# Optimization experiments

Hardware: AMD Instinct MI355X
Metric: run time of the kernel (lower is better)

The kernel has to match this reference:

```python
import jax, jax.numpy as jnp
import numpy as np

N = 50000      # nodes
E = 600000     # edges
DIN = 128      # dim_in
DOUT = 128     # dim_out (mulhead=1)
DG = 64        # dim_gate


def setup_inputs() -> dict:
    key = jax.random.key(0)
    ks = jax.random.split(key, 10)
    rows = jax.random.randint(ks[0], (E,), 0, N, dtype=jnp.int32)   # dest nodes
    cols = jax.random.randint(ks[1], (E,), 0, N, dtype=jnp.int32)   # src nodes
    vals = jax.random.uniform(ks[2], (E,), dtype=jnp.float32)       # adj_norm values
    feat = jax.random.normal(ks[3], (N, DIN), dtype=jnp.float32)
    s = 1.0 / np.sqrt(DIN)
    W0 = jax.random.normal(ks[4], (DIN, DOUT), dtype=jnp.float32) * s
    b0 = jnp.zeros((DOUT,), dtype=jnp.float32)
    W1 = jax.random.normal(ks[5], (DIN, DOUT), dtype=jnp.float32) * s
    b1 = jnp.zeros((DOUT,), dtype=jnp.float32)
    att = jax.random.normal(ks[6], (2 * DOUT,), dtype=jnp.float32) * 0.1  # attention param [1, 2*DOUT] flattened
    W_pool = jax.random.normal(ks[7], (DIN, DG), dtype=jnp.float32) * s    # weight_pool_gate
    W_gate = jax.random.normal(ks[8], (2 * DIN + DG, 1), dtype=jnp.float32) * 0.05  # weight_gate, mulhead=1
    offset0 = jnp.zeros((DOUT,), dtype=jnp.float32)
    scale0 = jnp.ones((DOUT,), dtype=jnp.float32)
    offset1 = jnp.zeros((DOUT,), dtype=jnp.float32)
    scale1 = jnp.ones((DOUT,), dtype=jnp.float32)
    return dict(rows=rows, cols=cols, vals=vals, feat=feat, W0=W0, b0=b0,
                W1=W1, b1=b1, att=att, W_pool=W_pool, W_gate=W_gate,
                offset0=offset0, scale0=scale0, offset1=offset1, scale1=scale1)


def _batch_norm(x, scale, offset):
    # per-node norm over the feature dim (unbiased=False), matching _batch_norm
    m = x.mean(axis=1, keepdims=True)
    v = x.var(axis=1, keepdims=True) + 1e-9
    return (x - m) * scale * jax.lax.rsqrt(v) + offset


def reference(rows, cols, vals, feat, W0, b0, W1, b1, att, W_pool, W_gate,
              offset0, scale0, offset1, scale1):
    n = feat.shape[0]
    d = W0.shape[1]
    # --- gate value (GaAN eq. 3) ---
    zj = feat @ W_pool                                   # [N, DG]
    neigh_zj = jax.ops.segment_max(zj[cols], rows, num_segments=n)  # per-row max over neighbors
    neigh_zj = jnp.where(jnp.isfinite(neigh_zj), neigh_zj, 0.0)     # empty rows -> zeros
    neigh_mean = jax.ops.segment_sum(vals[:, None] * feat[cols], rows, num_segments=n)  # spmm(adj, feat)
    gate = jnp.concatenate([feat, neigh_zj, neigh_mean], axis=1) @ W_gate  # [N, 1]
    # --- per-order feature transforms (order=1, mulhead=1) ---
    h0 = jax.nn.relu(feat @ W0 + b0)                     # order 0 (self)
    h1 = jax.nn.relu(feat @ W1 + b1)                     # order 1 (neighbor)
    # --- sparse attention aggregation ---
    a_self = jax.nn.leaky_relu(h0 @ att[:d], 0.2)        # [N]
    a_neigh = jax.nn.leaky_relu(h1 @ att[d:], 0.2)       # [N]
    e = a_self[rows] + a_neigh[cols]                     # per-edge score (replaces adj values)
    agg = jax.ops.segment_sum(e[:, None] * h1[cols], rows, num_segments=n)  # spmm(att_adj, h1)
    agg = agg * gate[:, :1]                              # gated
    # --- per-node batch norm, then 'mean' aggregation (sum of orders) ---
    return _batch_norm(h0, scale0, offset0) + _batch_norm(agg, scale1, offset1)
```

## Files before the change

kernel.cpp:

```cpp
#include <hip/hip_runtime.h>

#define DIN 128
#define DG 64

typedef __attribute__((ext_vector_type(8))) short short8;
typedef __attribute__((ext_vector_type(4))) float f32x4;

static __device__ __forceinline__ unsigned short f2bf(float x) {
    unsigned u = __builtin_bit_cast(unsigned, x);
    u = (u + 0x7FFF + ((u >> 16) & 1)) >> 16;
    return (unsigned short)u;
}
static __device__ __forceinline__ float bf2f(unsigned short s) {
    return __builtin_bit_cast(float, (unsigned)s << 16);
}
static __device__ __forceinline__ float bflo(unsigned u) {
    return __builtin_bit_cast(float, u << 16);
}
static __device__ __forceinline__ float bfhi(unsigned u) {
    return __builtin_bit_cast(float, u & 0xFFFF0000u);
}


#define AS_LD 132
#define ZJ_SMEM 25088

static __device__ __forceinline__ void zj_body(
    const float* __restrict__ feat, const float* __restrict__ Wp,
    const float* __restrict__ Wg,
    float* __restrict__ zjc, float* __restrict__ gpart, float* __restrict__ anf,
    int zb, int N, char* smem) {
    float* As = (float*)smem;
    float* Bs = (float*)(smem + 32 * AS_LD * 4);
    int tid = threadIdx.x;
    int tx = tid & 15, ty = tid >> 4;
    int m0 = zb * 128;
    if (m0 >= N) return;
    float acc[8][4];
    #pragma unroll
    for (int r = 0; r < 8; ++r)
        #pragma unroll
        for (int c = 0; c < 4; ++c) acc[r][c] = 0.f;
    float gdot[8], fdot[8];
    #pragma unroll
    for (int r = 0; r < 8; ++r) { gdot[r] = 0.f; fdot[r] = 0.f; }
    for (int kc = 0; kc < 128; kc += 32) {
        for (int i = tid; i < 1024; i += 256) {
            int m = i >> 3, kq = (i & 7) << 2;
            int node = m0 + m;
            float4 f;
            if (node < N) f = *(const float4*)&feat[(size_t)node * 128 + kc + kq];
            else          f = make_float4(0.f, 0.f, 0.f, 0.f);
            As[(kq + 0) * AS_LD + m] = f.x;
            As[(kq + 1) * AS_LD + m] = f.y;
            As[(kq + 2) * AS_LD + m] = f.z;
            As[(kq + 3) * AS_LD + m] = f.w;
        }
        for (int i = tid; i < 512; i += 256) {
            int k = i >> 4, cq = (i & 15) << 2;
            *(float4*)&Bs[k * 64 + cq] = *(const float4*)&Wp[(size_t)(kc + k) * 64 + cq];
        }
        __syncthreads();
        #pragma unroll 8
        for (int kk = 0; kk < 32; ++kk) {
            const float* ar = &As[kk * AS_LD];
            float4 a0 = *(const float4*)(ar + 4 * tx);
            float4 a1 = *(const float4*)(ar + 64 + 4 * tx);
            float4 b0v = *(const float4*)&Bs[kk * 64 + 4 * ty];
            float a[8] = {a0.x, a0.y, a0.z, a0.w, a1.x, a1.y, a1.z, a1.w};
            #pragma unroll
            for (int r = 0; r < 8; ++r) {
                acc[r][0] += a[r] * b0v.x; acc[r][1] += a[r] * b0v.y;
                acc[r][2] += a[r] * b0v.z; acc[r][3] += a[r] * b0v.w;
            }
            float g1 = Wg[kc + kk];
            float g2 = Wg[192 + kc + kk];
            #pragma unroll
            for (int r = 0; r < 8; ++r) { gdot[r] += a[r] * g1; fdot[r] += a[r] * g2; }
        }
        __syncthreads();
    }
    #pragma unroll
    for (int r = 0; r < 8; ++r) {
        int node = m0 + ((r < 4) ? (4 * tx + r) : (64 + 4 * tx + (r - 4)));
        if (node >= N) continue;
        *(float4*)&zjc[(size_t)node * 64 + 4 * ty] =
            make_float4(acc[r][0], acc[r][1], acc[r][2], acc[r][3]);
        if (ty == 0) { gpart[node] = gdot[r]; anf[2 * (size_t)node + 1] = fdot[r]; }
    }
}

__global__ void k_pre(const int* __restrict__ rows, int* __restrict__ deg,
                      int* __restrict__ slot, int E, int nDeg,
                      const float* __restrict__ W0, const float* __restrict__ W1,
                      unsigned short* __restrict__ Bt,
                      const float* __restrict__ feat, const float* __restrict__ Wp,
                      const float* __restrict__ Wg,
                      float* __restrict__ zjc, float* __restrict__ gpart,
                      float* __restrict__ anf, int N) {
    __shared__ __align__(16) char smem[ZJ_SMEM];
    int b = blockIdx.x;
    if (b < nDeg) {
        int e = b * 256 + threadIdx.x;
        if (e < E) slot[e] = atomicAdd(&deg[rows[e]], 1);
        return;
    }
    if (b < nDeg + 128) {
        int k = b - nDeg;
        int c = threadIdx.x;
        const float* W = (c < 128) ? W0 : W1;
        Bt[c * 128 + k] = f2bf(W[k * 128 + (c & 127)]);
        return;
    }
    zj_body(feat, Wp, Wg, zjc, gpart, anf, b - nDeg - 128, N, smem);
}

#define ALD 136
#define RED_OFF 32768
#define SMEM_BYTES 33792

static __device__ __forceinline__ void mfma_body(
    const float* __restrict__ feat, const unsigned short* __restrict__ Bt,
    const float* __restrict__ b0, const float* __restrict__ b1,
    const float* __restrict__ att, const float* __restrict__ zjc,
    float* __restrict__ h0, char* __restrict__ pack,
    float* __restrict__ anf, float* __restrict__ a_self, int N, char* smem) {
    unsigned short* Ah = (unsigned short*)smem;
    float* sredA = (float*)(smem + RED_OFF);
    float* nredA = sredA + 128;
    char* pb = smem;
    int tid = threadIdx.x;
    int m0 = blockIdx.x * 64;
    for (int i = tid; i < 2048; i += 256) {
        int row = i >> 5, ch = i & 31;
        int node = m0 + row;
        float4 f;
        if (node < N) f = *(const float4*)&feat[(size_t)node * 128 + ch * 4];
        else          f = make_float4(0.f, 0.f, 0.f, 0.f);
        unsigned p0 = (unsigned)f2bf(f.x) | ((unsigned)f2bf(f.y) << 16);
        unsigned p1 = (unsigned)f2bf(f.z) | ((unsigned)f2bf(f.w) << 16);
        *(uint2*)&Ah[row * ALD + ch * 4] = make_uint2(p0, p1);
    }
    __syncthreads();
    int w = tid >> 6, lane = tid & 63;
    int lm = lane & 15, q = lane >> 4;
    f32x4 acc[4][4];
    #pragma unroll
    for (int rt = 0; rt < 4; ++rt)
        #pragma unroll
        for (int ct = 0; ct < 4; ++ct)
            #pragma unroll
            for (int r = 0; r < 4; ++r) acc[rt][ct][r] = 0.f;
    #pragma unroll
    for (int ks = 0; ks < 4; ++ks) {
        short8 a[4], b[4];
        #pragma unroll
        for (int rt = 0; rt < 4; ++rt)
            a[rt] = *(const short8*)&Ah[(rt * 16 + lm) * ALD + ks * 32 + q * 8];
        #pragma unroll
        for (int ct = 0; ct < 4; ++ct)
            b[ct] = *(const short8*)&Bt[(size_t)(w * 64 + ct * 16 + lm) * 128 + ks * 32 + q * 8];
        #pragma unroll
        for (int rt = 0; rt < 4; ++rt)
            #pragma unroll
            for (int ct = 0; ct < 4; ++ct)
                acc[rt][ct] = __builtin_amdgcn_mfma_f32_16x16x32_bf16(a[rt], b[ct], acc[rt][ct], 0, 0, 0);
    }
    __syncthreads();

    float sacc[4][4];
    #pragma unroll
    for (int rt = 0; rt < 4; ++rt)
        #pragma unroll
        for (int r = 0; r < 4; ++r) sacc[rt][r] = 0.f;
    #pragma unroll
    for (int ct = 0; ct < 4; ++ct) {
        int col = w * 64 + ct * 16 + lm;
        float attc = att[col];
        float bias = (w < 2) ? b0[col] : b1[col - 128];
        int cp = col - 128;
        int pofs = (cp >> 2) * 16 + (cp & 3) * 2;
        #pragma unroll
        for (int rt = 0; rt < 4; ++rt) {
            #pragma unroll
            for (int r = 0; r < 4; ++r) {
                float v = acc[rt][ct][r] + bias;
                v = fmaxf(v, 0.f);
                sacc[rt][r] += v * attc;
                int row = rt * 16 + q * 4 + r;
                if (w < 2) {
                    int node = m0 + row;
                    if (node < N) h0[(size_t)node * 128 + col] = v;
                } else {
                    *(unsigned short*)(pb + row * 512 + pofs) = f2bf(v);
                }
            }
        }
    }
    for (int i = tid; i < 1024; i += 256) {
        int row = i >> 4, cq = i & 15;
        int node = m0 + row;
        float4 z;
        if (node < N) z = *(const float4*)&zjc[(size_t)node * 64 + cq * 4];
        else          z = make_float4(0.f, 0.f, 0.f, 0.f);
        char* prow = pb + row * 512 + cq * 32 + 8;
        *(float2*)(prow)      = make_float2(z.x, z.y);
        *(float2*)(prow + 16) = make_float2(z.z, z.w);
    }
    float* red = (w < 2) ? sredA : nredA;
    #pragma unroll
    for (int rt = 0; rt < 4; ++rt)
        #pragma unroll
        for (int r = 0; r < 4; ++r) {
            float s = sacc[rt][r];
            s += __shfl_xor(s, 1, 64); s += __shfl_xor(s, 2, 64);
            s += __shfl_xor(s, 4, 64); s += __shfl_xor(s, 8, 64);
            if (lm == 0) red[(w & 1) * 64 + rt * 16 + q * 4 + r] = s;
        }
    __syncthreads();
    for (int i = tid; i < 2048; i += 256) {
        float4 val = *(const float4*)(pb + i * 16);
        *(float4*)(pack + (size_t)(m0 + (i >> 5)) * 512 + (i & 31) * 16) = val;
    }
    if (tid < 64) {
        int node = m0 + tid;
        if (node < N) {
            float s  = sredA[tid] + sredA[64 + tid];
            float nn = nredA[tid] + nredA[64 + tid];
            a_self[node] = (s  >= 0.f) ? s  : 0.2f * s;
            anf[2 * (size_t)node] = (nn >= 0.f) ? nn : 0.2f * nn;
        }
    }
}

static __device__ __forceinline__ void scan_body(
    const int* __restrict__ deg, int* __restrict__ rowptr,
    unsigned long long* __restrict__ bstate, int n, int nbs, char* smem) {
    int b = blockIdx.x;
    if (b >= nbs) return;
    int* wsum = (int*)smem;
    int* bprefs = (int*)smem + 8;
    int tid = threadIdx.x, lane = tid & 63, w = tid >> 6;
    int base = b * 1024 + tid * 4;
    int4 v = make_int4(0, 0, 0, 0);
    if (base + 3 < n) v = *(const int4*)&deg[base];
    else {
        if (base     < n) v.x = deg[base];
        if (base + 1 < n) v.y = deg[base + 1];
        if (base + 2 < n) v.z = deg[base + 2];
        if (base + 3 < n) v.w = deg[base + 3];
    }
    int s = v.x + v.y + v.z + v.w;
    int x = s;
    #pragma unroll
    for (int off = 1; off < 64; off <<= 1) {
        int y = __shfl_up(x, off, 64);
        if (lane >= off) x += y;
    }
    if (lane == 63) wsum[w] = x;
    __syncthreads();
    int wpref = 0;
    for (int t = 0; t < w; ++t) wpref += wsum[t];
    int btotal = wsum[0] + wsum[1] + wsum[2] + wsum[3];
    int excl = x - s + wpref;
    if (tid == 0) {
        unsigned long long pk =
            ((unsigned long long)(b == 0 ? 2u : 1u) << 32) | (unsigned)btotal;
        atomicExch(&bstate[b], pk);
        int pref = 0;
        if (b > 0) {
            int i = b - 1;
            while (i >= 0) {
                unsigned long long st = atomicAdd(&bstate[i], 0ULL);
                unsigned f = (unsigned)(st >> 32);
                if (f == 0) { __builtin_amdgcn_s_sleep(1); continue; }
                pref += (int)(st & 0xffffffffULL);
                if (f == 2) break;
                --i;
            }
            atomicExch(&bstate[b], (2ULL << 32) | (unsigned)(pref + btotal));
        }
        bprefs[0] = pref;
    }
    __syncthreads();
    int p = bprefs[0] + excl;
    if (base + 3 < n) {
        *(int4*)&rowptr[base] = make_int4(p, p + v.x, p + v.x + v.y, p + v.x + v.y + v.z);
    } else {
        if (base     < n) rowptr[base]     = p;
        if (base + 1 < n) rowptr[base + 1] = p + v.x;
        if (base + 2 < n) rowptr[base + 2] = p + v.x + v.y;
        if (base + 3 < n) rowptr[base + 3] = p + v.x + v.y + v.z;
    }
    if (b == nbs - 1 && tid == 0) rowptr[n] = bprefs[0] + btotal;
}

__global__ __launch_bounds__(256) void k_fused(
    const float* __restrict__ feat, const unsigned short* __restrict__ Bt,
    const float* __restrict__ b0, const float* __restrict__ b1,
    const float* __restrict__ att, const float* __restrict__ zjc,
    float* __restrict__ h0, char* __restrict__ pack,
    float* __restrict__ anf, float* __restrict__ a_self,
    const int* __restrict__ deg, int* __restrict__ rowptr,
    unsigned long long* __restrict__ bstate, int nbs, int N) {
    __shared__ __align__(16) char smem[SMEM_BYTES];
    if (blockIdx.y == 0)
        mfma_body(feat, Bt, b0, b1, att, zjc, h0, pack, anf, a_self, N, smem);
    else
        scan_body(deg, rowptr, bstate, N, nbs, smem);
}

__global__ void k_scatter_meta(const int* __restrict__ rows, const int* __restrict__ cols,
                               const float* __restrict__ vals,
                               const int* __restrict__ rowptr, const int* __restrict__ slot,
                               const float* __restrict__ anf,
                               float4* __restrict__ meta, int E) {
    int e = blockIdx.x * blockDim.x + threadIdx.x;
    if (e < E) {
        int c = cols[e];
        int dst = rowptr[rows[e]] + slot[e];
        float2 av = *(const float2*)&anf[2 * (size_t)c];
        meta[dst] = make_float4(__builtin_bit_cast(float, c << 9),
                                av.x, vals[e] * av.y, 0.f);
    }
}

__global__ __launch_bounds__(256) void k_aggregate(
    const float4* __restrict__ meta, const int* __restrict__ rowptr,
    const float* __restrict__ h0, const char* __restrict__ pack,
    const float* __restrict__ a_self, const float* __restrict__ gpart,
    const float* __restrict__ Wg,
    const float* __restrict__ scale0, const float* __restrict__ offset0,
    const float* __restrict__ scale1, const float* __restrict__ offset1,
    float* __restrict__ out, int N) {
    int wid = threadIdx.x >> 6;
    int lane = threadIdx.x & 63;
    int sub = lane >> 5;
    int l = lane & 31;
    int r = blockIdx.x * 8 + wid * 2 + sub;
    int rr = (r < N) ? r : (N - 1);
    int jb = rowptr[rr], je = rowptr[rr + 1];
    int trips = (je - jb + 7) >> 3;
    int tother = __shfl_xor(trips, 32, 64);
    int tmax = (trips > tother) ? trips : tother;
    int jclamp = (je > 0) ? je - 1 : 0;
    float asr = a_self[rr];
    const char* packl = pack + l * 16;
    float4 acc = make_float4(0.f, 0.f, 0.f, 0.f);
    float2 zmax = make_float2(-__builtin_inff(), -__builtin_inff());
    float vfsum = 0.f;
    for (int t0 = 0; t0 < tmax; ++t0) {
        int j = jb + t0 * 8;
        int joff[8]; float esv[8];
        #pragma unroll
        for (int t = 0; t < 8; ++t) {
            int jj = j + t;
            bool a = jj < je;
            float4 mt = meta[a ? jj : jclamp];
            joff[t] = __builtin_bit_cast(int, mt.x);
            esv[t] = a ? (asr + mt.y) : 0.f;
            vfsum += a ? mt.z : 0.f;
        }
        uint4 v[8];
        #pragma unroll
        for (int t = 0; t < 8; ++t)
            v[t] = *(const uint4*)(packl + (size_t)(unsigned)joff[t]);
        #pragma unroll
        for (int t = 0; t < 8; ++t) {
            float e = esv[t];
            acc.x += e * bflo(v[t].x);
            acc.y += e * bfhi(v[t].x);
            acc.z += e * bflo(v[t].y);
            acc.w += e * bfhi(v[t].y);
            zmax.x = fmaxf(zmax.x, __builtin_bit_cast(float, v[t].z));
            zmax.y = fmaxf(zmax.y, __builtin_bit_cast(float, v[t].w));
        }
    }
    if (jb == je) { zmax.x = 0.f; zmax.y = 0.f; }
    float gs = zmax.x * Wg[128 + 2 * l] + zmax.y * Wg[129 + 2 * l];
    #pragma unroll
    for (int off = 16; off; off >>= 1) gs += __shfl_xor(gs, off, 64);
    float gate = gpart[rr] + gs + vfsum;
    float4 ag = make_float4(acc.x * gate, acc.y * gate, acc.z * gate, acc.w * gate);
    float4 x0 = ((const float4*)(h0 + (size_t)rr * 128))[l];
    float m0s = x0.x + x0.y + x0.z + x0.w;
    #pragma unroll
    for (int off = 16; off; off >>= 1) m0s += __shfl_xor(m0s, off, 64);
    float m0 = m0s * (1.f / 128.f);
    float4 d0 = make_float4(x0.x - m0, x0.y - m0, x0.z - m0, x0.w - m0);
    float v0s = d0.x * d0.x + d0.y * d0.y + d0.z * d0.z + d0.w * d0.w;
    #pragma unroll
    for (int off = 16; off; off >>= 1) v0s += __shfl_xor(v0s, off, 64);
    float inv0 = rsqrtf(v0s * (1.f / 128.f) + 1e-9f);
    float m1s = ag.x + ag.y + ag.z + ag.w;
    #pragma unroll
    for (int off = 16; off; off >>= 1) m1s += __shfl_xor(m1s, off, 64);
    float m1 = m1s * (1.f / 128.f);
    float4 d1 = make_float4(ag.x - m1, ag.y - m1, ag.z - m1, ag.w - m1);
    float v1s = d1.x * d1.x + d1.y * d1.y + d1.z * d1.z + d1.w * d1.w;
    #pragma unroll
    for (int off = 16; off; off >>= 1) v1s += __shfl_xor(v1s, off, 64);
    float inv1 = rsqrtf(v1s * (1.f / 128.f) + 1e-9f);
    if (r >= N) return;
    float4 sc0 = ((const float4*)scale0)[l], of0 = ((const float4*)offset0)[l];
    float4 sc1 = ((const float4*)scale1)[l], of1 = ((const float4*)offset1)[l];
    float4 o;
    o.x = d0.x * sc0.x * inv0 + of0.x + d1.x * sc1.x * inv1 + of1.x;
    o.y = d0.y * sc0.y * inv0 + of0.y + d1.y * sc1.y * inv1 + of1.y;
    o.z = d0.z * sc0.z * inv0 + of0.z + d1.z * sc1.z * inv1 + of1.z;
    o.w = d0.w * sc0.w * inv0 + of0.w + d1.w * sc1.w * inv1 + of1.w;
    ((float4*)(out + (size_t)r * 128))[l] = o;
}

extern "C" void kernel_launch(void* const* d_in, const int* in_sizes, int n_in,
                              void* d_out, int out_size, void* d_ws, size_t ws_size,
                              hipStream_t stream) {
    const int*   rows   = (const int*)d_in[0];
    const int*   cols   = (const int*)d_in[1];
    const float* vals   = (const float*)d_in[2];
    const float* feat   = (const float*)d_in[3];
    const float* W0     = (const float*)d_in[4];
    const float* b0     = (const float*)d_in[5];
    const float* W1     = (const float*)d_in[6];
    const float* b1     = (const float*)d_in[7];
    const float* att    = (const float*)d_in[8];
    const float* Wp     = (const float*)d_in[9];
    const float* Wg     = (const float*)d_in[10];
    const float* offset0 = (const float*)d_in[11];
    const float* scale0  = (const float*)d_in[12];
    const float* offset1 = (const float*)d_in[13];
    const float* scale1  = (const float*)d_in[14];
    float* out = (float*)d_out;

    const int E = in_sizes[0];
    const int N = in_sizes[3] / DIN;
    const int Npad = (N + 63) & ~63;

    char* ws = (char*)d_ws;
    float* h0          = (float*)ws;          ws += (size_t)N * 128 * sizeof(float);
    char* pack         = ws;                  ws += (size_t)Npad * 512;
    unsigned short* Bt = (unsigned short*)ws; ws += (size_t)256 * 128 * sizeof(unsigned short);
    float* a_self  = (float*)ws; ws += (size_t)N * sizeof(float);
    float* anf     = (float*)ws; ws += (size_t)N * 2 * sizeof(float);
    float* gpart   = (float*)ws; ws += (size_t)N * sizeof(float);
    float* zjc     = (float*)ws; ws += (size_t)N * 64 * sizeof(float);
    ws = (char*)(((size_t)ws + 7) & ~(size_t)7);
    unsigned long long* bstate = (unsigned long long*)ws; ws += 64 * sizeof(unsigned long long);
    int* deg      = (int*)ws; ws += (size_t)(N + 1) * sizeof(int);
    int* rowptr   = (int*)ws; ws += (size_t)(N + 1) * sizeof(int);
    int* slot     = (int*)ws; ws += (size_t)E * sizeof(int);
    ws = (char*)(((size_t)ws + 15) & ~(size_t)15);
    float4* meta  = (float4*)ws; ws += (size_t)E * sizeof(float4);

    hipMemsetAsync(bstate, 0, 64 * sizeof(unsigned long long) + (size_t)(N + 1) * sizeof(int), stream);

    int nDeg = (E + 255) / 256;
    int nZj = (N + 127) / 128;
    k_pre<<<nDeg + 128 + nZj, 256, 0, stream>>>(rows, deg, slot, E, nDeg, W0, W1, Bt,
                                                feat, Wp, Wg, zjc, gpart, anf, N);

    int nbs = (N + 1023) >> 10;
    dim3 gg(Npad / 64, 2);
    k_fused<<<gg, 256, 0, stream>>>(feat, Bt, b0, b1, att, zjc,
                                    h0, pack, anf, a_self,
                                    deg, rowptr, bstate, nbs, N);

    k_scatter_meta<<<nDeg, 256, 0, stream>>>(rows, cols, vals, rowptr, slot,
                                             anf, meta, E);

    int nb8 = (N + 7) / 8;
    k_aggregate<<<nb8, 256, 0, stream>>>(meta, rowptr, h0, pack,
                                         a_self, gpart, Wg,
                                         scale0, offset0, scale1, offset1, out, N);
}
```

Baseline: 266.7 us.

## Privatize degree counters into eight copies to reduce atomic contention

The edge degree-count atomics now go to one of eight per-block-group copies of the degree array, and the scan combines them and emits per-copy base offsets that scatter_meta uses to place edges. This spreads atomic traffic over more addresses, and edge counting moves out of the combined prep kernel into its own launch. The cost is a larger memset, eight times the degree reads and base writes in the scan, one extra kernel launch, and a changed edge order within each row.

```diff
diff --git a/kernel.cpp b/kernel.cpp
--- a/kernel.cpp
+++ b/kernel.cpp
@@ -90,29 +90,30 @@
     }
 }
 
-__global__ void k_pre(const int* __restrict__ rows, int* __restrict__ deg,
-                      int* __restrict__ slot, int E, int nDeg,
-                      const float* __restrict__ W0, const float* __restrict__ W1,
-                      unsigned short* __restrict__ Bt,
-                      const float* __restrict__ feat, const float* __restrict__ Wp,
-                      const float* __restrict__ Wg,
-                      float* __restrict__ zjc, float* __restrict__ gpart,
-                      float* __restrict__ anf, int N) {
+__global__ void k_prep(const float* __restrict__ W0, const float* __restrict__ W1,
+                       unsigned short* __restrict__ Bt,
+                       const float* __restrict__ feat, const float* __restrict__ Wp,
+                       const float* __restrict__ Wg,
+                       float* __restrict__ zjc, float* __restrict__ gpart,
+                       float* __restrict__ anf, int N) {
     __shared__ __align__(16) char smem[ZJ_SMEM];
     int b = blockIdx.x;
-    if (b < nDeg) {
-        int e = b * 256 + threadIdx.x;
-        if (e < E) slot[e] = atomicAdd(&deg[rows[e]], 1);
-        return;
-    }
-    if (b < nDeg + 128) {
-        int k = b - nDeg;
+    if (b < 128) {
+        int k = b;
         int c = threadIdx.x;
         const float* W = (c < 128) ? W0 : W1;
         Bt[c * 128 + k] = f2bf(W[k * 128 + (c & 127)]);
         return;
     }
-    zj_body(feat, Wp, Wg, zjc, gpart, anf, b - nDeg - 128, N, smem);
+    zj_body(feat, Wp, Wg, zjc, gpart, anf, b - 128, N, smem);
+}
+
+__global__ void k_edges(const int* __restrict__ rows, int* __restrict__ deg8,
+                        int* __restrict__ slot, int E, int N) {
+    int b = blockIdx.x;
+    int e = b * 256 + threadIdx.x;
+    if (e < E)
+        slot[e] = atomicAdd(&deg8[(size_t)(b & 7) * N + rows[e]], 1);
 }
 
 #define ALD 136
@@ -234,7 +235,8 @@
 }
 
 static __device__ __forceinline__ void scan_body(
-    const int* __restrict__ deg, int* __restrict__ rowptr,
+    const int* __restrict__ deg8, int* __restrict__ rowptr,
+    int* __restrict__ base8,
     unsigned long long* __restrict__ bstate, int n, int nbs, char* smem) {
     int b = blockIdx.x;
     if (b >= nbs) return;
@@ -242,13 +244,25 @@
     int* bprefs = (int*)smem + 8;
     int tid = threadIdx.x, lane = tid & 63, w = tid >> 6;
     int base = b * 1024 + tid * 4;
+    int4 d[8];
     int4 v = make_int4(0, 0, 0, 0);
-    if (base + 3 < n) v = *(const int4*)&deg[base];
-    else {
-        if (base     < n) v.x = deg[base];
-        if (base + 1 < n) v.y = deg[base + 1];
-        if (base + 2 < n) v.z = deg[base + 2];
-        if (base + 3 < n) v.w = deg[base + 3];
+    bool full = (base + 3 < n);
+    if (full) {
+        #pragma unroll
+        for (int x = 0; x < 8; ++x) {
+            d[x] = *(const int4*)&deg8[(size_t)x * n + base];
+            v.x += d[x].x; v.y += d[x].y; v.z += d[x].z; v.w += d[x].w;
+        }
+    } else {
+        #pragma unroll
+        for (int x = 0; x < 8; ++x) {
+            d[x] = make_int4(0, 0, 0, 0);
+            if (base     < n) d[x].x = deg8[(size_t)x * n + base];
+            if (base + 1 < n) d[x].y = deg8[(size_t)x * n + base + 1];
+            if (base + 2 < n) d[x].z = deg8[(size_t)x * n + base + 2];
+            if (base + 3 < n) d[x].w = deg8[(size_t)x * n + base + 3];
+            v.x += d[x].x; v.y += d[x].y; v.z += d[x].z; v.w += d[x].w;
+        }
     }
     int s = v.x + v.y + v.z + v.w;
     int x = s;
@@ -284,13 +298,29 @@
     }
     __syncthreads();
     int p = bprefs[0] + excl;
-    if (base + 3 < n) {
-        *(int4*)&rowptr[base] = make_int4(p, p + v.x, p + v.x + v.y, p + v.x + v.y + v.z);
+    int4 racc = make_int4(p, p + v.x, p + v.x + v.y, p + v.x + v.y + v.z);
+    if (full) {
+        *(int4*)&rowptr[base] = racc;
+        #pragma unroll
+        for (int xx = 0; xx < 8; ++xx) {
+            *(int4*)&base8[(size_t)xx * n + base] = racc;
+            racc.x += d[xx].x; racc.y += d[xx].y;
+            racc.z += d[xx].z; racc.w += d[xx].w;
+        }
     } else {
-        if (base     < n) rowptr[base]     = p;
-        if (base + 1 < n) rowptr[base + 1] = p + v.x;
-        if (base + 2 < n) rowptr[base + 2] = p + v.x + v.y;
-        if (base + 3 < n) rowptr[base + 3] = p + v.x + v.y + v.z;
+        int pr[4] = {racc.x, racc.y, racc.z, racc.w};
+        int dv[4];
+        for (int i = 0; i < 4; ++i) {
+            if (base + i >= n) break;
+            rowptr[base + i] = pr[i];
+            int run = pr[i];
+            #pragma unroll
+            for (int xx = 0; xx < 8; ++xx) {
+                base8[(size_t)xx * n + base + i] = run;
+                dv[0] = (i == 0) ? d[xx].x : (i == 1) ? d[xx].y : (i == 2) ? d[xx].z : d[xx].w;
+                run += dv[0];
+            }
+        }
     }
     if (b == nbs - 1 && tid == 0) rowptr[n] = bprefs[0] + btotal;
 }
@@ -301,24 +331,25 @@
     const float* __restrict__ att, const float* __restrict__ zjc,
     float* __restrict__ h0, char* __restrict__ pack,
     float* __restrict__ anf, float* __restrict__ a_self,
-    const int* __restrict__ deg, int* __restrict__ rowptr,
+    const int* __restrict__ deg8, int* __restrict__ rowptr,
+    int* __restrict__ base8,
     unsigned long long* __restrict__ bstate, int nbs, int N) {
     __shared__ __align__(16) char smem[SMEM_BYTES];
     if (blockIdx.y == 0)
         mfma_body(feat, Bt, b0, b1, att, zjc, h0, pack, anf, a_self, N, smem);
     else
-        scan_body(deg, rowptr, bstate, N, nbs, smem);
+        scan_body(deg8, rowptr, base8, bstate, N, nbs, smem);
 }
 
 __global__ void k_scatter_meta(const int* __restrict__ rows, const int* __restrict__ cols,
                                const float* __restrict__ vals,
-                               const int* __restrict__ rowptr, const int* __restrict__ slot,
+                               const int* __restrict__ base8, const int* __restrict__ slot,
                                const float* __restrict__ anf,
-                               float4* __restrict__ meta, int E) {
+                               float4* __restrict__ meta, int E, int N) {
     int e = blockIdx.x * blockDim.x + threadIdx.x;
     if (e < E) {
         int c = cols[e];
-        int dst = rowptr[rows[e]] + slot[e];
+        int dst = base8[(size_t)((e >> 8) & 7) * N + rows[e]] + slot[e];
         float2 av = *(const float2*)&anf[2 * (size_t)c];
         meta[dst] = make_float4(__builtin_bit_cast(float, c << 9),
                                 av.x, vals[e] * av.y, 0.f);
@@ -446,27 +477,30 @@
     float* zjc     = (float*)ws; ws += (size_t)N * 64 * sizeof(float);
     ws = (char*)(((size_t)ws + 7) & ~(size_t)7);
     unsigned long long* bstate = (unsigned long long*)ws; ws += 64 * sizeof(unsigned long long);
-    int* deg      = (int*)ws; ws += (size_t)(N + 1) * sizeof(int);
+    int* deg8     = (int*)ws; ws += (size_t)8 * N * sizeof(int);
     int* rowptr   = (int*)ws; ws += (size_t)(N + 1) * sizeof(int);
+    int* base8    = (int*)ws; ws += (size_t)8 * N * sizeof(int);
     int* slot     = (int*)ws; ws += (size_t)E * sizeof(int);
     ws = (char*)(((size_t)ws + 15) & ~(size_t)15);
     float4* meta  = (float4*)ws; ws += (size_t)E * sizeof(float4);
 
-    hipMemsetAsync(bstate, 0, 64 * sizeof(unsigned long long) + (size_t)(N + 1) * sizeof(int), stream);
+    hipMemsetAsync(bstate, 0,
+                   64 * sizeof(unsigned long long) + (size_t)8 * N * sizeof(int), stream);
+
+    int nZj = (N + 127) / 128;
+    k_prep<<<128 + nZj, 256, 0, stream>>>(W0, W1, Bt, feat, Wp, Wg, zjc, gpart, anf, N);
 
     int nDeg = (E + 255) / 256;
-    int nZj = (N + 127) / 128;
-    k_pre<<<nDeg + 128 + nZj, 256, 0, stream>>>(rows, deg, slot, E, nDeg, W0, W1, Bt,
-                                                feat, Wp, Wg, zjc, gpart, anf, N);
+    k_edges<<<nDeg, 256, 0, stream>>>(rows, deg8, slot, E, N);
 
     int nbs = (N + 1023) >> 10;
     dim3 gg(Npad / 64, 2);
     k_fused<<<gg, 256, 0, stream>>>(feat, Bt, b0, b1, att, zjc,
                                     h0, pack, anf, a_self,
-                                    deg, rowptr, bstate, nbs, N);
-
-    k_scatter_meta<<<nDeg, 256, 0, stream>>>(rows, cols, vals, rowptr, slot,
-                                             anf, meta, E);
+                                    deg8, rowptr, base8, bstate, nbs, N);
+
+    k_scatter_meta<<<nDeg, 256, 0, stream>>>(rows, cols, vals, base8, slot,
+                                             anf, meta, E, N);
 
     int nb8 = (N + 7) / 8;
     k_aggregate<<<nb8, 256, 0, stream>>>(meta, rowptr, h0, pack,
```

Measured after the change: 254.0 us. 1.05x faster.
